# Kernel tuning notes

Hardware: AMD Instinct MI355X
Metric: run time of the kernel (lower is better)

## Reference

```python
import jax, jax.numpy as jnp
import numpy as np

# Static sizes
B, P, D = 256, 32, 128            # graphs, patches/graph, hidden
N, NS = 200_000, 500_000          # original nodes, combined-subgraph nodes
ES, EO = 1_000_000, 400_000       # combined-subgraph edges, original edges
RW, PRW = 20, 8                   # rw_dim, patch_rw_dim
NL_GNN, NL_MIX = 4, 2
TH, CH = 64, 512                  # mixer token-hidden, channel-hidden
ATOM_V, BOND_V = 128, 8


def seg_sum(x, idx, n):
    return jax.ops.segment_sum(x, idx, num_segments=n)


def seg_mean(x, idx, n):
    s = seg_sum(x, idx, n)
    c = seg_sum(jnp.ones((idx.shape[0], 1), x.dtype), idx, n)
    return s / jnp.maximum(c, 1.0)


def ln(x, g, b):
    m = x.mean(-1, keepdims=True)
    v = x.var(-1, keepdims=True)
    return (x - m) * jax.lax.rsqrt(v + 1e-5) * g + b


def setup_inputs() -> dict:
    key = jax.random.key(0)
    ks = iter(jax.random.split(key, 48))

    def nrm(shape, scale=0.05):
        return jax.random.normal(next(ks), shape, jnp.float32) * scale

    inp = {
        "x_atom": jax.random.randint(next(ks), (N,), 0, ATOM_V),
        "rw_pos_enc": jax.random.normal(next(ks), (N, RW), jnp.float32),
        "edge_attr": jax.random.randint(next(ks), (EO,), 0, BOND_V),
        "nodes_mapper": jax.random.randint(next(ks), (NS,), 0, N),
        "edges_mapper": jax.random.randint(next(ks), (ES,), 0, EO),
        "edge_index": jax.random.randint(next(ks), (2, ES), 0, NS),
        "batch_x": jax.random.randint(next(ks), (NS,), 0, B * P),
        "patch_pe": jax.random.normal(next(ks), (B * P, PRW), jnp.float32),
        "mask": jnp.ones((B, P), dtype=bool),
        # parameters
        "atom_emb": nrm((ATOM_V, D)),
        "bond_emb": nrm((BOND_V, D)),
        "rw_W": nrm((RW, D)), "rw_b": jnp.zeros((D,), jnp.float32),
        "prw_W": nrm((PRW, D)), "prw_b": jnp.zeros((D,), jnp.float32),
        "gnn_W": nrm((NL_GNN, D, D)), "gnn_b": jnp.zeros((NL_GNN, D), jnp.float32),
        "U_W": nrm((NL_GNN - 1, D, D)), "U_b": jnp.zeros((NL_GNN - 1, D), jnp.float32),
        "ln1_g": jnp.ones((NL_MIX, D), jnp.float32), "ln1_b": jnp.zeros((NL_MIX, D), jnp.float32),
        "tW1": nrm((NL_MIX, P, TH)), "tb1": jnp.zeros((NL_MIX, TH), jnp.float32),
        "tW2": nrm((NL_MIX, TH, P)), "tb2": jnp.zeros((NL_MIX, P), jnp.float32),
        "ln2_g": jnp.ones((NL_MIX, D), jnp.float32), "ln2_b": jnp.zeros((NL_MIX, D), jnp.float32),
        "cW1": nrm((NL_MIX, D, CH)), "cb1": jnp.zeros((NL_MIX, CH), jnp.float32),
        "cW2": nrm((NL_MIX, CH, D)), "cb2": jnp.zeros((NL_MIX, D), jnp.float32),
        "oW1": nrm((D, D)), "ob1": jnp.zeros((D,), jnp.float32),
        "oW2": nrm((D, 1)), "ob2": jnp.zeros((1,), jnp.float32),
    }
    return inp


def reference(x_atom, rw_pos_enc, edge_attr, nodes_mapper, edges_mapper, edge_index,
              batch_x, patch_pe, mask, atom_emb, bond_emb, rw_W, rw_b, prw_W, prw_b,
              gnn_W, gnn_b, U_W, U_b, ln1_g, ln1_b, tW1, tb1, tW2, tb2,
              ln2_g, ln2_b, cW1, cb1, cW2, cb2, oW1, ob1, oW2, ob2):
    # node / edge encoders
    x = atom_emb[x_atom] + rw_pos_enc @ rw_W + rw_b          # [N, D]
    e = bond_emb[edge_attr][edges_mapper]                    # [ES, D]
    x = x[nodes_mapper]                                      # [NS, D]
    src, dst = edge_index[0], edge_index[1]

    for i in range(NL_GNN):
        if i > 0:
            # patch-pool -> broadcast back, mix, then sync copies of same node
            sub = seg_mean(x, batch_x, B * P)[batch_x]
            x = x + jax.nn.relu(sub @ U_W[i - 1] + U_b[i - 1])
            x = seg_mean(x, nodes_mapper, N)[nodes_mapper]
        # GINE-style conv: msg = relu(x_src + e), sum-aggregate, MLP, residual
        msg = jax.nn.relu(x[src] + e)                        # [ES, D]
        agg = seg_sum(msg, dst, NS)                          # [NS, D]
        x = x + jax.nn.relu((x + agg) @ gnn_W[i] + gnn_b[i])

    sx = seg_mean(x, batch_x, B * P) + patch_pe @ prw_W + prw_b   # [B*P, D]
    m = sx.reshape(B, P, D)

    for l in range(NL_MIX):
        # token mixing
        y = ln(m, ln1_g[l], ln1_b[l]).transpose(0, 2, 1)     # [B, D, P]
        y = jax.nn.gelu(y @ tW1[l] + tb1[l]) @ tW2[l] + tb2[l]
        m = m + y.transpose(0, 2, 1)
        # channel mixing
        y = ln(m, ln2_g[l], ln2_b[l])
        m = m + (jax.nn.gelu(y @ cW1[l] + cb1[l]) @ cW2[l] + cb2[l])

    mf = mask.astype(jnp.float32)
    pooled = (m * mf[:, :, None]).sum(1) / mf.sum(1, keepdims=True)  # [B, D]
    return jax.nn.relu(pooled @ oW1 + ob1) @ oW2 + ob2              # [B, 1]
```

## Files before the change

kernel.cpp:

```cpp
#include <hip/hip_runtime.h>
#include <hip/hip_bf16.h>
#include <math.h>

#define N_ORIG 200000
#define NS_    500000
#define ES_    1000000
#define B_     256
#define P_     32
#define D_     128
#define BP_    8192
#define RW_    20
#define PRW_   8
#define TH_    64
#define CH_    512

static inline int cdiv_l(long a, long b){ return (int)((a + b - 1) / b); }

typedef unsigned short ushort_t;
typedef __attribute__((ext_vector_type(8))) short gmx_bv8;
typedef __attribute__((ext_vector_type(4))) float gmx_fv4;

__device__ __forceinline__ float b2f(ushort_t u){
    union { unsigned int i; float f; } c; c.i = ((unsigned int)u) << 16; return c.f;
}
__device__ __forceinline__ ushort_t f2b(float f){
    union { float f; unsigned int u; } c; c.f = f;
    unsigned int u = c.u;
    u += 0x7fffu + ((u >> 16) & 1u);
    return (ushort_t)(u >> 16);
}
__device__ __forceinline__ float4 b2f4(ushort4 v){
    return make_float4(b2f(v.x), b2f(v.y), b2f(v.z), b2f(v.w));
}
__device__ __forceinline__ ushort4 f2b4(float4 v){
    ushort4 r; r.x = f2b(v.x); r.y = f2b(v.y); r.z = f2b(v.z); r.w = f2b(v.w); return r;
}

__device__ __forceinline__ float gelu_t(float x){
    float t = tanhf(0.7978845608028654f * (x + 0.044715f * x * x * x));
    return 0.5f * x * (1.0f + t);
}

__global__ void k_breadcrumb(float* __restrict__ out, int n, float v){
    int i = blockIdx.x * 256 + threadIdx.x;
    if (i < n) out[i] = v;
}

__global__ void k_deg_edges(const int* __restrict__ dstv, const int* __restrict__ perm,
                            int* __restrict__ deg){
    int e = blockIdx.x * 256 + threadIdx.x;
    if (e >= ES_) return;
    atomicAdd(&deg[perm[dstv[e]]], 1);
}

__global__ void k_deg_ns(const int* __restrict__ bx, const int* __restrict__ nm,
                         int* __restrict__ pdeg, int* __restrict__ ndeg){
    int i = blockIdx.x * 256 + threadIdx.x;
    if (i >= NS_) return;
    atomicAdd(&pdeg[bx[i]], 1);
    atomicAdd(&ndeg[nm[i]], 1);
}

__global__ __launch_bounds__(256)
void k_scan1(int* __restrict__ a, int* __restrict__ bsum, int n){
    __shared__ int sb[256];
    int tid = threadIdx.x;
    long base = (long)blockIdx.x * 1024 + tid * 4;
    int v0 = 0, v1 = 0, v2 = 0, v3 = 0;
    if (base + 0 < n) v0 = a[base + 0];
    if (base + 1 < n) v1 = a[base + 1];
    if (base + 2 < n) v2 = a[base + 2];
    if (base + 3 < n) v3 = a[base + 3];
    int tsum = v0 + v1 + v2 + v3;
    sb[tid] = tsum;
    __syncthreads();
    for (int o = 1; o < 256; o <<= 1){
        int t = (tid >= o) ? sb[tid - o] : 0;
        __syncthreads();
        sb[tid] += t;
        __syncthreads();
    }
    int excl = sb[tid] - tsum;
    if (tid == 255) bsum[blockIdx.x] = sb[255];
    if (base + 0 < n) a[base + 0] = excl;
    if (base + 1 < n) a[base + 1] = excl + v0;
    if (base + 2 < n) a[base + 2] = excl + v0 + v1;
    if (base + 3 < n) a[base + 3] = excl + v0 + v1 + v2;
}

__global__ __launch_bounds__(512)
void k_scan2(int* __restrict__ bsum, int nb){
    __shared__ int sb[512];
    int tid = threadIdx.x;
    int orig = (tid < nb) ? bsum[tid] : 0;
    sb[tid] = orig;
    __syncthreads();
    for (int o = 1; o < 512; o <<= 1){
        int t = (tid >= o) ? sb[tid - o] : 0;
        __syncthreads();
        sb[tid] += t;
        __syncthreads();
    }
    if (tid < nb) bsum[tid] = sb[tid] - orig;
}

__global__ void k_scan3(int* __restrict__ a, const int* __restrict__ bsum,
                        int* __restrict__ cursor, int n, int total){
    long i = (long)blockIdx.x * 256 + threadIdx.x;
    if (i < n){
        int v = a[i] + bsum[i >> 10];
        a[i] = v;
        cursor[i] = v;
    } else if (i == n){
        a[n] = total;
    }
}

__global__ void k_scatter_ns(const int* __restrict__ bx, const int* __restrict__ nm,
                             int* __restrict__ cur_p, int* __restrict__ cur_n,
                             int* __restrict__ perm, int* __restrict__ bx2,
                             int* __restrict__ nm2, int* __restrict__ nlist){
    int i = blockIdx.x * 256 + threadIdx.x;
    if (i >= NS_) return;
    int b = bx[i], n = nm[i];
    int pp = atomicAdd(&cur_p[b], 1);
    perm[i] = pp;
    bx2[pp] = b;
    nm2[pp] = n;
    int pn = atomicAdd(&cur_n[n], 1);
    nlist[pn] = pp;
}

__global__ void k_scatter_edges(const int* __restrict__ srcv, const int* __restrict__ dstv,
                                const int* __restrict__ ea, const int* __restrict__ em,
                                const int* __restrict__ nm, const int* __restrict__ perm,
                                int* __restrict__ cursor, int* __restrict__ epack){
    int e = blockIdx.x * 256 + threadIdx.x;
    if (e >= ES_) return;
    int nd = perm[dstv[e]];
    int pos = atomicAdd(&cursor[nd], 1);
    epack[pos] = nm[srcv[e]] | (ea[em[e]] << 18);
}

__global__ void k_encode(const int* __restrict__ xa, const float* __restrict__ rw,
                         const float* __restrict__ aemb, const float* __restrict__ rwW,
                         const float* __restrict__ rwb, ushort_t* __restrict__ xn){
    long i = (long)blockIdx.x * 256 + threadIdx.x;
    if (i >= (long)N_ORIG * 32) return;
    int n = (int)(i >> 5), q = (int)(i & 31);
    const float4* aemb4 = (const float4*)aemb;
    const float4* rwW4  = (const float4*)rwW;
    const float4* rwb4  = (const float4*)rwb;
    float4 v = aemb4[(long)xa[n] * 32 + q];
    float4 bb = rwb4[q];
    v.x += bb.x; v.y += bb.y; v.z += bb.z; v.w += bb.w;
    const float* rr = rw + (long)n * RW_;
    #pragma unroll
    for (int k = 0; k < RW_; k++){
        float rv = rr[k];
        float4 ww = rwW4[k * 32 + q];
        v.x = fmaf(rv, ww.x, v.x); v.y = fmaf(rv, ww.y, v.y);
        v.z = fmaf(rv, ww.z, v.z); v.w = fmaf(rv, ww.w, v.w);
    }
    ((ushort4*)xn)[i] = f2b4(v);
}

__global__ __launch_bounds__(128)
void k_patch_pool(const ushort_t* __restrict__ xs, const int* __restrict__ prp,
                  ushort_t* __restrict__ pm){
    int p = blockIdx.x, d = threadIdx.x;
    int j0 = prp[p], j1 = prp[p + 1];
    float s0 = 0.f, s1 = 0.f;
    int j = j0;
    for (; j + 1 < j1; j += 2){
        s0 += b2f(xs[(long)j * D_ + d]);
        s1 += b2f(xs[(long)(j + 1) * D_ + d]);
    }
    if (j < j1) s0 += b2f(xs[(long)j * D_ + d]);
    pm[(long)p * D_ + d] = f2b((s0 + s1) / fmaxf((float)(j1 - j0), 1.f));
}

__global__ __launch_bounds__(128)
void k_patch_pool_sx(const ushort_t* __restrict__ xs, const int* __restrict__ prp,
                     const float* __restrict__ ppe, const float* __restrict__ pW,
                     const float* __restrict__ pb, float* __restrict__ m){
    int p = blockIdx.x, d = threadIdx.x;
    int j0 = prp[p], j1 = prp[p + 1];
    float s0 = 0.f, s1 = 0.f;
    int j = j0;
    for (; j + 1 < j1; j += 2){
        s0 += b2f(xs[(long)j * D_ + d]);
        s1 += b2f(xs[(long)(j + 1) * D_ + d]);
    }
    if (j < j1) s0 += b2f(xs[(long)j * D_ + d]);
    float s = (s0 + s1) / fmaxf((float)(j1 - j0), 1.f) + pb[d];
    #pragma unroll
    for (int k = 0; k < PRW_; k++) s = fmaf(ppe[p * PRW_ + k], pW[k * D_ + d], s);
    m[(long)p * D_ + d] = s;
}

__global__ __launch_bounds__(128)
void k_node_resync(const ushort_t* __restrict__ xs, const ushort_t* __restrict__ subT,
                   const int* __restrict__ bx2, const int* __restrict__ nrp,
                   const int* __restrict__ nlist, ushort_t* __restrict__ xn){
    int n = blockIdx.x, d = threadIdx.x;
    int j0 = nrp[n], j1 = nrp[n + 1];
    float s = 0.f;
    int j = j0;
    for (; j + 2 <= j1; j += 2){
        int ra = nlist[j], rb = nlist[j + 1];
        int ba = bx2[ra], bb_ = bx2[rb];
        float va = b2f(xs[(long)ra * D_ + d]);
        float vb = b2f(xs[(long)rb * D_ + d]);
        float ua = b2f(subT[(long)ba * D_ + d]);
        float ub = b2f(subT[(long)bb_ * D_ + d]);
        s += va + ua + vb + ub;
    }
    if (j < j1){
        int ra = nlist[j];
        int ba = bx2[ra];
        s += b2f(xs[(long)ra * D_ + d]) + b2f(subT[(long)ba * D_ + d]);
    }
    xn[(long)n * D_ + d] = f2b(s / fmaxf((float)(j1 - j0), 1.f));
}

__global__ __launch_bounds__(256)
void k_gemm_mfma(const ushort_t* __restrict__ in, const float* __restrict__ W,
                 const float* __restrict__ bvec, ushort_t* __restrict__ out, int nrows){
    __shared__ char sInB[16 * 256];
    int tid = threadIdx.x;
    int wid = tid >> 6, lane = tid & 63;
    int colA = lane & 15, rgrp = lane >> 4;
    int c0 = 32 * wid + colA, c1 = c0 + 16;
    float bias0 = bvec[c0], bias1 = bvec[c1];
    union { gmx_bv8 v; short s[8]; } bf0[4], bf1[4];
    #pragma unroll
    for (int kb = 0; kb < 4; kb++){
        int kr = kb * 32 + 8 * rgrp;
        #pragma unroll
        for (int j = 0; j < 8; j++){
            bf0[kb].s[j] = (short)f2b(W[(kr + j) * D_ + c0]);
            bf1[kb].s[j] = (short)f2b(W[(kr + j) * D_ + c1]);
        }
    }
    const ushort4* in4 = (const ushort4*)in;
    int ntiles = nrows >> 4;
    for (int tile = blockIdx.x; tile < ntiles; tile += gridDim.x){
        int r0 = tile * 16;
        #pragma unroll
        for (int it = 0; it < 2; it++){
            int k = tid + it * 256;
            int r = k >> 5, q = k & 31;
            ushort4 v = in4[(long)(r0 + r) * 32 + q];
            int off = (r * 256 + q * 8) ^ ((r & 7) << 4);
            *(ushort4*)&sInB[off] = v;
        }
        __syncthreads();
        gmx_fv4 acc0 = {0.f,0.f,0.f,0.f}, acc1 = {0.f,0.f,0.f,0.f};
        #pragma unroll
        for (int kb = 0; kb < 4; kb++){
            int kslot = kb * 4 + rgrp;
            gmx_bv8 a = *(const gmx_bv8*)&sInB[(colA * 256 + kslot * 16) ^ ((colA & 7) << 4)];
            acc0 = __builtin_amdgcn_mfma_f32_16x16x32_bf16(a, bf0[kb].v, acc0, 0, 0, 0);
            acc1 = __builtin_amdgcn_mfma_f32_16x16x32_bf16(a, bf1[kb].v, acc1, 0, 0, 0);
        }
        #pragma unroll
        for (int ri = 0; ri < 4; ri++){
            long base = (long)(r0 + rgrp * 4 + ri) * D_;
            out[base + c0] = f2b(fmaxf(acc0[ri] + bias0, 0.f));
            out[base + c1] = f2b(fmaxf(acc1[ri] + bias1, 0.f));
        }
        __syncthreads();
    }
}

#define CROWS 16

__global__ __launch_bounds__(256)
void k_conv_mfma(const ushort_t* __restrict__ xn, const int* __restrict__ nm2,
                 ushort_t* __restrict__ xout,
                 const int* __restrict__ rp, const int* __restrict__ epack,
                 const float* __restrict__ bond, const float* __restrict__ W,
                 const float* __restrict__ bvec){
    __shared__ char sInB[CROWS * 256];
    __shared__ ushort_t sSelf[CROWS * D_];
    __shared__ int sRp[CROWS + 1];
    __shared__ int sEp[256];
    int tid = threadIdx.x;
    int wid = tid >> 6, lane = tid & 63;
    int colA = lane & 15, rgrp = lane >> 4;
    int c0 = 32 * wid + colA, c1 = c0 + 16;
    float bias0 = bvec[c0], bias1 = bvec[c1];
    union { gmx_bv8 v; short s[8]; } bf0[4], bf1[4];
    #pragma unroll
    for (int kb = 0; kb < 4; kb++){
        int kr = kb * 32 + 8 * rgrp;
        #pragma unroll
        for (int j = 0; j < 8; j++){
            bf0[kb].s[j] = (short)f2b(W[(kr + j) * D_ + c0]);
            bf1[kb].s[j] = (short)f2b(W[(kr + j) * D_ + c1]);
        }
    }
    const ushort4* xn4 = (const ushort4*)xn;
    const float4* bond4 = (const float4*)bond;
    const int ntiles = NS_ / CROWS;
    for (int tile = blockIdx.x; tile < ntiles; tile += gridDim.x){
        int r0 = tile * CROWS;
        if (tid < CROWS + 1) sRp[tid] = rp[r0 + tid];
        __syncthreads();
        int eb0 = sRp[0];
        int ne = sRp[CROWS] - eb0;
        int nc = ne < 256 ? ne : 256;
        for (int k2 = tid; k2 < nc; k2 += 256) sEp[k2] = epack[eb0 + k2];
        __syncthreads();
        #pragma unroll
        for (int it = 0; it < 2; it++){
            int k = tid + it * 256;
            int r = k >> 5, q = k & 31;
            ushort4 selfb = xn4[(long)nm2[r0 + r] * 32 + q];
            *(ushort4*)&sSelf[r * D_ + q * 4] = selfb;
            float4 v = b2f4(selfb);
            int e0 = sRp[r], e1 = sRp[r + 1];
            int e = e0;
            for (; e + 2 <= e1; e += 2){
                int i0 = e - eb0;
                int pk0 = (i0 < 256) ? sEp[i0] : epack[e];
                int pk1 = (i0 + 1 < 256) ? sEp[i0 + 1] : epack[e + 1];
                float4 u0 = b2f4(xn4[(long)(pk0 & 0x3FFFF) * 32 + q]);
                float4 u1 = b2f4(xn4[(long)(pk1 & 0x3FFFF) * 32 + q]);
                float4 b0 = bond4[((pk0 >> 18) & 7) * 32 + q];
                float4 b1 = bond4[((pk1 >> 18) & 7) * 32 + q];
                v.x += fmaxf(u0.x + b0.x, 0.f) + fmaxf(u1.x + b1.x, 0.f);
                v.y += fmaxf(u0.y + b0.y, 0.f) + fmaxf(u1.y + b1.y, 0.f);
                v.z += fmaxf(u0.z + b0.z, 0.f) + fmaxf(u1.z + b1.z, 0.f);
                v.w += fmaxf(u0.w + b0.w, 0.f) + fmaxf(u1.w + b1.w, 0.f);
            }
            if (e < e1){
                int i0 = e - eb0;
                int pk0 = (i0 < 256) ? sEp[i0] : epack[e];
                float4 u0 = b2f4(xn4[(long)(pk0 & 0x3FFFF) * 32 + q]);
                float4 b0 = bond4[((pk0 >> 18) & 7) * 32 + q];
                v.x += fmaxf(u0.x + b0.x, 0.f);
                v.y += fmaxf(u0.y + b0.y, 0.f);
                v.z += fmaxf(u0.z + b0.z, 0.f);
                v.w += fmaxf(u0.w + b0.w, 0.f);
            }
            int off = (r * 256 + q * 8) ^ ((r & 7) << 4);
            *(ushort4*)&sInB[off] = f2b4(v);
        }
        __syncthreads();
        gmx_fv4 acc0 = {0.f,0.f,0.f,0.f}, acc1 = {0.f,0.f,0.f,0.f};
        #pragma unroll
        for (int kb = 0; kb < 4; kb++){
            int kslot = kb * 4 + rgrp;
            gmx_bv8 a = *(const gmx_bv8*)&sInB[(colA * 256 + kslot * 16) ^ ((colA & 7) << 4)];
            acc0 = __builtin_amdgcn_mfma_f32_16x16x32_bf16(a, bf0[kb].v, acc0, 0, 0, 0);
            acc1 = __builtin_amdgcn_mfma_f32_16x16x32_bf16(a, bf1[kb].v, acc1, 0, 0, 0);
        }
        #pragma unroll
        for (int ri = 0; ri < 4; ri++){
            int prow = rgrp * 4 + ri;
            long base = (long)(r0 + prow) * D_;
            float o0 = b2f(sSelf[prow * D_ + c0]) + fmaxf(acc0[ri] + bias0, 0.f);
            float o1 = b2f(sSelf[prow * D_ + c1]) + fmaxf(acc1[ri] + bias1, 0.f);
            xout[base + c0] = f2b(o0);
            xout[base + c1] = f2b(o1);
        }
        __syncthreads();
    }
}

__global__ __launch_bounds__(256)
void k_token_mix(float* __restrict__ m, const float* __restrict__ g, const float* __restrict__ be,
                 const float* __restrict__ tW1, const float* __restrict__ tb1,
                 const float* __restrict__ tW2, const float* __restrict__ tb2){
    __shared__ float sy[P_][D_];
    __shared__ float sh[D_][TH_ + 1];
    int b = blockIdx.x, tid = threadIdx.x;
    float* mb = m + (long)b * P_ * D_;
    int wv = tid >> 6, ln_ = tid & 63;
    for (int r = wv; r < P_; r += 4){
        float v0 = mb[r * D_ + ln_], v1 = mb[r * D_ + 64 + ln_];
        float s = v0 + v1, ss = v0 * v0 + v1 * v1;
        #pragma unroll
        for (int o = 32; o > 0; o >>= 1){ s += __shfl_down(s, o, 64); ss += __shfl_down(ss, o, 64); }
        s = __shfl(s, 0, 64); ss = __shfl(ss, 0, 64);
        float mu = s * (1.f / 128.f);
        float var = ss * (1.f / 128.f) - mu * mu;
        float rs = rsqrtf(var + 1e-5f);
        sy[r][ln_]      = (v0 - mu) * rs * g[ln_]      + be[ln_];
        sy[r][64 + ln_] = (v1 - mu) * rs * g[64 + ln_] + be[64 + ln_];
    }
    __syncthreads();
    for (int o = tid; o < D_ * TH_; o += 256){
        int t = o & 63, d = o >> 6;
        float a = tb1[t];
        #pragma unroll
        for (int p = 0; p < P_; p++) a = fmaf(sy[p][d], tW1[p * TH_ + t], a);
        sh[d][t] = gelu_t(a);
    }
    __syncthreads();
    for (int o = tid; o < P_ * D_; o += 256){
        int d = o & 127, p = o >> 7;
        float a = tb2[p];
        #pragma unroll
        for (int t = 0; t < TH_; t++) a = fmaf(sh[d][t], tW2[t * P_ + p], a);
        mb[p * D_ + d] += a;
    }
}

__global__ __launch_bounds__(256)
void k_channel_mix(float* __restrict__ m, const float* __restrict__ g, const float* __restrict__ be,
                   const float* __restrict__ cW1, const float* __restrict__ cb1,
                   const float* __restrict__ cW2, const float* __restrict__ cb2){
    __shared__ float sy[16][D_];
    __shared__ float sh[16][CH_ + 1];
    int r0 = blockIdx.x * 16, tid = threadIdx.x;
    int wv = tid >> 6, ln_ = tid & 63;
    for (int r = wv; r < 16; r += 4){
        float v0 = m[(long)(r0 + r) * D_ + ln_], v1 = m[(long)(r0 + r) * D_ + 64 + ln_];
        float s = v0 + v1, ss = v0 * v0 + v1 * v1;
        #pragma unroll
        for (int o = 32; o > 0; o >>= 1){ s += __shfl_down(s, o, 64); ss += __shfl_down(ss, o, 64); }
        s = __shfl(s, 0, 64); ss = __shfl(ss, 0, 64);
        float mu = s * (1.f / 128.f);
        float var = ss * (1.f / 128.f) - mu * mu;
        float rs = rsqrtf(var + 1e-5f);
        sy[r][ln_]      = (v0 - mu) * rs * g[ln_]      + be[ln_];
        sy[r][64 + ln_] = (v1 - mu) * rs * g[64 + ln_] + be[64 + ln_];
    }
    __syncthreads();
    #pragma unroll
    for (int th = 0; th < 2; th++){
        int t = tid + th * 256;
        float acc[16];
        #pragma unroll
        for (int r = 0; r < 16; r++) acc[r] = cb1[t];
        for (int k = 0; k < D_; k++){
            float w = cW1[k * CH_ + t];
            #pragma unroll
            for (int r = 0; r < 16; r++) acc[r] = fmaf(sy[r][k], w, acc[r]);
        }
        #pragma unroll
        for (int r = 0; r < 16; r++) sh[r][t] = gelu_t(acc[r]);
    }
    __syncthreads();
    {
        int d = tid & 127, rbase = tid >> 7;
        float acc[8];
        #pragma unroll
        for (int q = 0; q < 8; q++) acc[q] = 0.f;
        for (int t = 0; t < CH_; t++){
            float w = cW2[t * D_ + d];
            #pragma unroll
            for (int q = 0; q < 8; q++) acc[q] = fmaf(sh[rbase + 2 * q][t], w, acc[q]);
        }
        float cb = cb2[d];
        #pragma unroll
        for (int q = 0; q < 8; q++){
            int row = r0 + rbase + 2 * q;
            m[(long)row * D_ + d] += acc[q] + cb;
        }
    }
}

__global__ __launch_bounds__(128)
void k_final(const float* __restrict__ m, const float* __restrict__ oW1, const float* __restrict__ ob1,
             const float* __restrict__ oW2, const float* __restrict__ ob2, float* __restrict__ out){
    __shared__ float sp[D_];
    __shared__ float red[128];
    int b = blockIdx.x, tid = threadIdx.x;
    float a = 0.f;
    for (int p = 0; p < P_; p++) a += m[(long)b * P_ * D_ + p * D_ + tid];
    sp[tid] = a * (1.0f / P_);
    __syncthreads();
    float h = ob1[tid];
    for (int d = 0; d < D_; d++) h = fmaf(sp[d], oW1[d * D_ + tid], h);
    h = fmaxf(h, 0.f) * oW2[tid];
    red[tid] = h;
    __syncthreads();
    for (int s = 64; s > 0; s >>= 1){
        if (tid < s) red[tid] += red[tid + s];
        __syncthreads();
    }
    if (tid == 0) out[b] = red[0] + ob2[0];
}

extern "C" void kernel_launch(void* const* d_in, const int* in_sizes, int n_in,
                              void* d_out, int out_size, void* d_ws, size_t ws_size,
                              hipStream_t stream){
    const int*   x_atom       = (const int*)  d_in[0];
    const float* rw_pe        = (const float*)d_in[1];
    const int*   edge_attr    = (const int*)  d_in[2];
    const int*   nodes_mapper = (const int*)  d_in[3];
    const int*   edges_mapper = (const int*)  d_in[4];
    const int*   edge_index   = (const int*)  d_in[5];
    const int*   batch_x      = (const int*)  d_in[6];
    const float* patch_pe     = (const float*)d_in[7];
    const float* atom_emb = (const float*)d_in[9];
    const float* bond_emb = (const float*)d_in[10];
    const float* rw_W  = (const float*)d_in[11];
    const float* rw_b  = (const float*)d_in[12];
    const float* prw_W = (const float*)d_in[13];
    const float* prw_b = (const float*)d_in[14];
    const float* gnn_W = (const float*)d_in[15];
    const float* gnn_b = (const float*)d_in[16];
    const float* U_W   = (const float*)d_in[17];
    const float* U_b   = (const float*)d_in[18];
    const float* ln1_g = (const float*)d_in[19];
    const float* ln1_b = (const float*)d_in[20];
    const float* tW1   = (const float*)d_in[21];
    const float* tb1   = (const float*)d_in[22];
    const float* tW2   = (const float*)d_in[23];
    const float* tb2   = (const float*)d_in[24];
    const float* ln2_g = (const float*)d_in[25];
    const float* ln2_b = (const float*)d_in[26];
    const float* cW1   = (const float*)d_in[27];
    const float* cb1   = (const float*)d_in[28];
    const float* cW2   = (const float*)d_in[29];
    const float* cb2   = (const float*)d_in[30];
    const float* oW1   = (const float*)d_in[31];
    const float* ob1   = (const float*)d_in[32];
    const float* oW2   = (const float*)d_in[33];
    const float* ob2   = (const float*)d_in[34];

    const int* srcv = edge_index;
    const int* dstv = edge_index + ES_;

    char* w = (char*)d_ws;
    size_t offXS  = 0;
    size_t offXN  = offXS  + (size_t)NS_ * D_ * 2;
    size_t offRP  = offXN  + (size_t)N_ORIG * D_ * 2;
    size_t offEP  = offRP  + 2000064;
    size_t offPRP = offEP  + (size_t)ES_ * 4;
    size_t offNRP = offPRP + 32832;
    size_t offNL  = offNRP + 800064;
    size_t offPERM= offNL  + (size_t)NS_ * 4;
    size_t offBX2 = offPERM+ (size_t)NS_ * 4;
    size_t offNM2 = offBX2 + (size_t)NS_ * 4;
    size_t offBS  = offNM2 + (size_t)NS_ * 4;
    size_t offPM  = offBS  + 2048;
    size_t offST  = offPM  + (size_t)BP_ * D_ * 2;
    size_t offM   = offST  + (size_t)BP_ * D_ * 2;
    size_t needed = offM   + (size_t)BP_ * D_ * 4;

    if (ws_size < needed){
        k_breadcrumb<<<cdiv_l(out_size, 256), 256, 0, stream>>>((float*)d_out, out_size,
                                                                (float)(ws_size >> 20));
        return;
    }

    k_breadcrumb<<<cdiv_l(out_size, 256), 256, 0, stream>>>((float*)d_out, out_size, 7.0f);

    ushort_t* xs = (ushort_t*)(w + offXS);
    ushort_t* xn = (ushort_t*)(w + offXN);
    int* rp    = (int*)(w + offRP);
    int* ep    = (int*)(w + offEP);
    int* prp   = (int*)(w + offPRP);
    int* nrp   = (int*)(w + offNRP);
    int* nlist = (int*)(w + offNL);
    int* perm  = (int*)(w + offPERM);
    int* bx2   = (int*)(w + offBX2);
    int* nm2   = (int*)(w + offNM2);
    int* bsum  = (int*)(w + offBS);
    ushort_t* pm   = (ushort_t*)(w + offPM);
    ushort_t* subT = (ushort_t*)(w + offST);
    float*    mbuf = (float*)(w + offM);
    int* cur_e = (int*)(w + offXS);
    int* cur_p = (int*)(w + offXS + 4194304);
    int* cur_n = (int*)(w + offXS + 8388608);

    const int TPB = 256;

    hipMemsetAsync(prp, 0, 32832, stream);
    hipMemsetAsync(nrp, 0, 800064, stream);
    k_deg_ns<<<cdiv_l(NS_, TPB), TPB, 0, stream>>>(batch_x, nodes_mapper, prp, nrp);
    k_scan1<<<cdiv_l(BP_, 1024), TPB, 0, stream>>>(prp, bsum, BP_);
    k_scan2<<<1, 512, 0, stream>>>(bsum, cdiv_l(BP_, 1024));
    k_scan3<<<cdiv_l(BP_ + 1, TPB), TPB, 0, stream>>>(prp, bsum, cur_p, BP_, NS_);
    k_scan1<<<cdiv_l(N_ORIG, 1024), TPB, 0, stream>>>(nrp, bsum, N_ORIG);
    k_scan2<<<1, 512, 0, stream>>>(bsum, cdiv_l(N_ORIG, 1024));
    k_scan3<<<cdiv_l(N_ORIG + 1, TPB), TPB, 0, stream>>>(nrp, bsum, cur_n, N_ORIG, NS_);
    k_scatter_ns<<<cdiv_l(NS_, TPB), TPB, 0, stream>>>(batch_x, nodes_mapper, cur_p, cur_n,
                                                       perm, bx2, nm2, nlist);
    hipMemsetAsync(rp, 0, 2000064, stream);
    k_deg_edges<<<cdiv_l(ES_, TPB), TPB, 0, stream>>>(dstv, perm, rp);
    k_scan1<<<cdiv_l(NS_, 1024), TPB, 0, stream>>>(rp, bsum, NS_);
    k_scan2<<<1, 512, 0, stream>>>(bsum, cdiv_l(NS_, 1024));
    k_scan3<<<cdiv_l(NS_ + 1, TPB), TPB, 0, stream>>>(rp, bsum, cur_e, NS_, ES_);
    k_scatter_edges<<<cdiv_l(ES_, TPB), TPB, 0, stream>>>(srcv, dstv, edge_attr, edges_mapper,
                                                          nodes_mapper, perm, cur_e, ep);

    k_encode<<<cdiv_l((long)N_ORIG * 32, TPB), TPB, 0, stream>>>(x_atom, rw_pe, atom_emb,
                                                                 rw_W, rw_b, xn);

    for (int i = 0; i < 4; i++){
        if (i > 0){
            k_patch_pool<<<BP_, 128, 0, stream>>>(xs, prp, pm);
            k_gemm_mfma<<<256, TPB, 0, stream>>>(pm, U_W + (i - 1) * D_ * D_,
                                                 U_b + (i - 1) * D_, subT, BP_);
            k_node_resync<<<N_ORIG, 128, 0, stream>>>(xs, subT, bx2, nrp, nlist, xn);
        }
        k_conv_mfma<<<2048, TPB, 0, stream>>>(xn, nm2, xs, rp, ep, bond_emb,
                                              gnn_W + i * D_ * D_, gnn_b + i * D_);
    }

    k_patch_pool_sx<<<BP_, 128, 0, stream>>>(xs, prp, patch_pe, prw_W, prw_b, mbuf);

    for (int l = 0; l < 2; l++){
        k_token_mix<<<B_, TPB, 0, stream>>>(mbuf, ln1_g + l * D_, ln1_b + l * D_,
                                            tW1 + l * P_ * TH_, tb1 + l * TH_,
                                            tW2 + l * TH_ * P_, tb2 + l * P_);
        k_channel_mix<<<BP_ / 16, TPB, 0, stream>>>(mbuf, ln2_g + l * D_, ln2_b + l * D_,
                                                    cW1 + l * D_ * CH_, cb1 + l * CH_,
                                                    cW2 + l * CH_ * D_, cb2 + l * D_);
    }
    k_final<<<B_, 128, 0, stream>>>(mbuf, oW1, ob1, oW2, ob2, (float*)d_out);
}
```

Before: 1.676 ms.

## Order subgraph nodes by original node and fuse patch pooling into GEMM

Subgraph node rows are now permuted so that copies of the same original node sit next to each other. This makes the node resync read contiguous rows, while patch pooling gathers rows through a new per-patch index list. Patch pooling and the U GEMM are fused into one kernel that pools 16 patches into shared memory and multiplies them with MFMA, which removes the intermediate pooled buffer and one launch. The cost moves to indirect gathers in patch pooling, and the edge CSR ordering by destination changes as well, which may alter locality in the conv kernel.

```diff
diff --git a/kernel.cpp b/kernel.cpp
--- a/kernel.cpp
+++ b/kernel.cpp
@@ -119,16 +119,16 @@
 __global__ void k_scatter_ns(const int* __restrict__ bx, const int* __restrict__ nm,
                              int* __restrict__ cur_p, int* __restrict__ cur_n,
                              int* __restrict__ perm, int* __restrict__ bx2,
-                             int* __restrict__ nm2, int* __restrict__ nlist){
+                             int* __restrict__ nm2, int* __restrict__ plist){
     int i = blockIdx.x * 256 + threadIdx.x;
     if (i >= NS_) return;
     int b = bx[i], n = nm[i];
+    int pn = atomicAdd(&cur_n[n], 1);
+    perm[i] = pn;
+    bx2[pn] = b;
+    nm2[pn] = n;
     int pp = atomicAdd(&cur_p[b], 1);
-    perm[i] = pp;
-    bx2[pp] = b;
-    nm2[pp] = n;
-    int pn = atomicAdd(&cur_n[n], 1);
-    nlist[pn] = pp;
+    plist[pp] = pn;
 }
 
 __global__ void k_scatter_edges(const int* __restrict__ srcv, const int* __restrict__ dstv,
@@ -165,69 +165,12 @@
     ((ushort4*)xn)[i] = f2b4(v);
 }
 
-__global__ __launch_bounds__(128)
-void k_patch_pool(const ushort_t* __restrict__ xs, const int* __restrict__ prp,
-                  ushort_t* __restrict__ pm){
-    int p = blockIdx.x, d = threadIdx.x;
-    int j0 = prp[p], j1 = prp[p + 1];
-    float s0 = 0.f, s1 = 0.f;
-    int j = j0;
-    for (; j + 1 < j1; j += 2){
-        s0 += b2f(xs[(long)j * D_ + d]);
-        s1 += b2f(xs[(long)(j + 1) * D_ + d]);
-    }
-    if (j < j1) s0 += b2f(xs[(long)j * D_ + d]);
-    pm[(long)p * D_ + d] = f2b((s0 + s1) / fmaxf((float)(j1 - j0), 1.f));
-}
-
-__global__ __launch_bounds__(128)
-void k_patch_pool_sx(const ushort_t* __restrict__ xs, const int* __restrict__ prp,
-                     const float* __restrict__ ppe, const float* __restrict__ pW,
-                     const float* __restrict__ pb, float* __restrict__ m){
-    int p = blockIdx.x, d = threadIdx.x;
-    int j0 = prp[p], j1 = prp[p + 1];
-    float s0 = 0.f, s1 = 0.f;
-    int j = j0;
-    for (; j + 1 < j1; j += 2){
-        s0 += b2f(xs[(long)j * D_ + d]);
-        s1 += b2f(xs[(long)(j + 1) * D_ + d]);
-    }
-    if (j < j1) s0 += b2f(xs[(long)j * D_ + d]);
-    float s = (s0 + s1) / fmaxf((float)(j1 - j0), 1.f) + pb[d];
-    #pragma unroll
-    for (int k = 0; k < PRW_; k++) s = fmaf(ppe[p * PRW_ + k], pW[k * D_ + d], s);
-    m[(long)p * D_ + d] = s;
-}
-
-__global__ __launch_bounds__(128)
-void k_node_resync(const ushort_t* __restrict__ xs, const ushort_t* __restrict__ subT,
-                   const int* __restrict__ bx2, const int* __restrict__ nrp,
-                   const int* __restrict__ nlist, ushort_t* __restrict__ xn){
-    int n = blockIdx.x, d = threadIdx.x;
-    int j0 = nrp[n], j1 = nrp[n + 1];
-    float s = 0.f;
-    int j = j0;
-    for (; j + 2 <= j1; j += 2){
-        int ra = nlist[j], rb = nlist[j + 1];
-        int ba = bx2[ra], bb_ = bx2[rb];
-        float va = b2f(xs[(long)ra * D_ + d]);
-        float vb = b2f(xs[(long)rb * D_ + d]);
-        float ua = b2f(subT[(long)ba * D_ + d]);
-        float ub = b2f(subT[(long)bb_ * D_ + d]);
-        s += va + ua + vb + ub;
-    }
-    if (j < j1){
-        int ra = nlist[j];
-        int ba = bx2[ra];
-        s += b2f(xs[(long)ra * D_ + d]) + b2f(subT[(long)ba * D_ + d]);
-    }
-    xn[(long)n * D_ + d] = f2b(s / fmaxf((float)(j1 - j0), 1.f));
-}
-
 __global__ __launch_bounds__(256)
-void k_gemm_mfma(const ushort_t* __restrict__ in, const float* __restrict__ W,
-                 const float* __restrict__ bvec, ushort_t* __restrict__ out, int nrows){
+void k_pool_gemm(const ushort_t* __restrict__ xs, const int* __restrict__ prp,
+                 const int* __restrict__ plist, const float* __restrict__ W,
+                 const float* __restrict__ bvec, ushort_t* __restrict__ out){
     __shared__ char sInB[16 * 256];
+    __shared__ int sPrp[17];
     int tid = threadIdx.x;
     int wid = tid >> 6, lane = tid & 63;
     int colA = lane & 15, rgrp = lane >> 4;
@@ -243,35 +186,89 @@
             bf1[kb].s[j] = (short)f2b(W[(kr + j) * D_ + c1]);
         }
     }
-    const ushort4* in4 = (const ushort4*)in;
-    int ntiles = nrows >> 4;
-    for (int tile = blockIdx.x; tile < ntiles; tile += gridDim.x){
-        int r0 = tile * 16;
-        #pragma unroll
-        for (int it = 0; it < 2; it++){
-            int k = tid + it * 256;
-            int r = k >> 5, q = k & 31;
-            ushort4 v = in4[(long)(r0 + r) * 32 + q];
-            int off = (r * 256 + q * 8) ^ ((r & 7) << 4);
-            *(ushort4*)&sInB[off] = v;
-        }
-        __syncthreads();
-        gmx_fv4 acc0 = {0.f,0.f,0.f,0.f}, acc1 = {0.f,0.f,0.f,0.f};
-        #pragma unroll
-        for (int kb = 0; kb < 4; kb++){
-            int kslot = kb * 4 + rgrp;
-            gmx_bv8 a = *(const gmx_bv8*)&sInB[(colA * 256 + kslot * 16) ^ ((colA & 7) << 4)];
-            acc0 = __builtin_amdgcn_mfma_f32_16x16x32_bf16(a, bf0[kb].v, acc0, 0, 0, 0);
-            acc1 = __builtin_amdgcn_mfma_f32_16x16x32_bf16(a, bf1[kb].v, acc1, 0, 0, 0);
-        }
-        #pragma unroll
-        for (int ri = 0; ri < 4; ri++){
-            long base = (long)(r0 + rgrp * 4 + ri) * D_;
-            out[base + c0] = f2b(fmaxf(acc0[ri] + bias0, 0.f));
-            out[base + c1] = f2b(fmaxf(acc1[ri] + bias1, 0.f));
-        }
-        __syncthreads();
-    }
+    int p0 = blockIdx.x * 16;
+    if (tid < 17) sPrp[tid] = prp[p0 + tid];
+    __syncthreads();
+    const ushort4* xs4 = (const ushort4*)xs;
+    #pragma unroll
+    for (int it = 0; it < 2; it++){
+        int k = tid + it * 256;
+        int r = k >> 5, q = k & 31;
+        int j0 = sPrp[r], j1 = sPrp[r + 1];
+        float4 s0 = make_float4(0.f,0.f,0.f,0.f), s1 = make_float4(0.f,0.f,0.f,0.f);
+        int j = j0;
+        for (; j + 2 <= j1; j += 2){
+            float4 a = b2f4(xs4[(long)plist[j] * 32 + q]);
+            float4 b = b2f4(xs4[(long)plist[j + 1] * 32 + q]);
+            s0.x += a.x; s0.y += a.y; s0.z += a.z; s0.w += a.w;
+            s1.x += b.x; s1.y += b.y; s1.z += b.z; s1.w += b.w;
+        }
+        if (j < j1){
+            float4 a = b2f4(xs4[(long)plist[j] * 32 + q]);
+            s0.x += a.x; s0.y += a.y; s0.z += a.z; s0.w += a.w;
+        }
+        float inv = 1.f / fmaxf((float)(j1 - j0), 1.f);
+        float4 v = make_float4((s0.x + s1.x) * inv, (s0.y + s1.y) * inv,
+                               (s0.z + s1.z) * inv, (s0.w + s1.w) * inv);
+        int off = (r * 256 + q * 8) ^ ((r & 7) << 4);
+        *(ushort4*)&sInB[off] = f2b4(v);
+    }
+    __syncthreads();
+    gmx_fv4 acc0 = {0.f,0.f,0.f,0.f}, acc1 = {0.f,0.f,0.f,0.f};
+    #pragma unroll
+    for (int kb = 0; kb < 4; kb++){
+        int kslot = kb * 4 + rgrp;
+        gmx_bv8 a = *(const gmx_bv8*)&sInB[(colA * 256 + kslot * 16) ^ ((colA & 7) << 4)];
+        acc0 = __builtin_amdgcn_mfma_f32_16x16x32_bf16(a, bf0[kb].v, acc0, 0, 0, 0);
+        acc1 = __builtin_amdgcn_mfma_f32_16x16x32_bf16(a, bf1[kb].v, acc1, 0, 0, 0);
+    }
+    #pragma unroll
+    for (int ri = 0; ri < 4; ri++){
+        long base = (long)(p0 + rgrp * 4 + ri) * D_;
+        out[base + c0] = f2b(fmaxf(acc0[ri] + bias0, 0.f));
+        out[base + c1] = f2b(fmaxf(acc1[ri] + bias1, 0.f));
+    }
+}
+
+__global__ __launch_bounds__(128)
+void k_patch_pool_sx(const ushort_t* __restrict__ xs, const int* __restrict__ prp,
+                     const int* __restrict__ plist, const float* __restrict__ ppe,
+                     const float* __restrict__ pW, const float* __restrict__ pb,
+                     float* __restrict__ m){
+    int p = blockIdx.x, d = threadIdx.x;
+    int j0 = prp[p], j1 = prp[p + 1];
+    float s0 = 0.f, s1 = 0.f;
+    int j = j0;
+    for (; j + 2 <= j1; j += 2){
+        s0 += b2f(xs[(long)plist[j] * D_ + d]);
+        s1 += b2f(xs[(long)plist[j + 1] * D_ + d]);
+    }
+    if (j < j1) s0 += b2f(xs[(long)plist[j] * D_ + d]);
+    float s = (s0 + s1) / fmaxf((float)(j1 - j0), 1.f) + pb[d];
+    #pragma unroll
+    for (int k = 0; k < PRW_; k++) s = fmaf(ppe[p * PRW_ + k], pW[k * D_ + d], s);
+    m[(long)p * D_ + d] = s;
+}
+
+__global__ __launch_bounds__(128)
+void k_node_resync(const ushort_t* __restrict__ xs, const ushort_t* __restrict__ subT,
+                   const int* __restrict__ bx2, const int* __restrict__ nrp,
+                   ushort_t* __restrict__ xn){
+    int n = blockIdx.x, d = threadIdx.x;
+    int j0 = nrp[n], j1 = nrp[n + 1];
+    float s = 0.f;
+    int j = j0;
+    for (; j + 2 <= j1; j += 2){
+        float va = b2f(xs[(long)j * D_ + d]);
+        float vb = b2f(xs[(long)(j + 1) * D_ + d]);
+        float ua = b2f(subT[(long)bx2[j] * D_ + d]);
+        float ub = b2f(subT[(long)bx2[j + 1] * D_ + d]);
+        s += va + ua + vb + ub;
+    }
+    if (j < j1){
+        s += b2f(xs[(long)j * D_ + d]) + b2f(subT[(long)bx2[j] * D_ + d]);
+    }
+    xn[(long)n * D_ + d] = f2b(s / fmaxf((float)(j1 - j0), 1.f));
 }
 
 #define CROWS 16
@@ -534,13 +531,12 @@
     size_t offEP  = offRP  + 2000064;
     size_t offPRP = offEP  + (size_t)ES_ * 4;
     size_t offNRP = offPRP + 32832;
-    size_t offNL  = offNRP + 800064;
-    size_t offPERM= offNL  + (size_t)NS_ * 4;
+    size_t offPL  = offNRP + 800064;
+    size_t offPERM= offPL  + (size_t)NS_ * 4;
     size_t offBX2 = offPERM+ (size_t)NS_ * 4;
     size_t offNM2 = offBX2 + (size_t)NS_ * 4;
     size_t offBS  = offNM2 + (size_t)NS_ * 4;
-    size_t offPM  = offBS  + 2048;
-    size_t offST  = offPM  + (size_t)BP_ * D_ * 2;
+    size_t offST  = offBS  + 2048;
     size_t offM   = offST  + (size_t)BP_ * D_ * 2;
     size_t needed = offM   + (size_t)BP_ * D_ * 4;
 
@@ -558,12 +554,11 @@
     int* ep    = (int*)(w + offEP);
     int* prp   = (int*)(w + offPRP);
     int* nrp   = (int*)(w + offNRP);
-    int* nlist = (int*)(w + offNL);
+    int* plist = (int*)(w + offPL);
     int* perm  = (int*)(w + offPERM);
     int* bx2   = (int*)(w + offBX2);
     int* nm2   = (int*)(w + offNM2);
     int* bsum  = (int*)(w + offBS);
-    ushort_t* pm   = (ushort_t*)(w + offPM);
     ushort_t* subT = (ushort_t*)(w + offST);
     float*    mbuf = (float*)(w + offM);
     int* cur_e = (int*)(w + offXS);
@@ -582,7 +577,7 @@
     k_scan2<<<1, 512, 0, stream>>>(bsum, cdiv_l(N_ORIG, 1024));
     k_scan3<<<cdiv_l(N_ORIG + 1, TPB), TPB, 0, stream>>>(nrp, bsum, cur_n, N_ORIG, NS_);
     k_scatter_ns<<<cdiv_l(NS_, TPB), TPB, 0, stream>>>(batch_x, nodes_mapper, cur_p, cur_n,
-                                                       perm, bx2, nm2, nlist);
+                                                       perm, bx2, nm2, plist);
     hipMemsetAsync(rp, 0, 2000064, stream);
     k_deg_edges<<<cdiv_l(ES_, TPB), TPB, 0, stream>>>(dstv, perm, rp);
     k_scan1<<<cdiv_l(NS_, 1024), TPB, 0, stream>>>(rp, bsum, NS_);
@@ -596,16 +591,16 @@
 
     for (int i = 0; i < 4; i++){
         if (i > 0){
-            k_patch_pool<<<BP_, 128, 0, stream>>>(xs, prp, pm);
-            k_gemm_mfma<<<256, TPB, 0, stream>>>(pm, U_W + (i - 1) * D_ * D_,
-                                                 U_b + (i - 1) * D_, subT, BP_);
-            k_node_resync<<<N_ORIG, 128, 0, stream>>>(xs, subT, bx2, nrp, nlist, xn);
+            k_pool_gemm<<<BP_ / 16, TPB, 0, stream>>>(xs, prp, plist,
+                                                      U_W + (i - 1) * D_ * D_,
+                                                      U_b + (i - 1) * D_, subT);
+            k_node_resync<<<N_ORIG, 128, 0, stream>>>(xs, subT, bx2, nrp, xn);
         }
         k_conv_mfma<<<2048, TPB, 0, stream>>>(xn, nm2, xs, rp, ep, bond_emb,
                                               gnn_W + i * D_ * D_, gnn_b + i * D_);
     }
 
-    k_patch_pool_sx<<<BP_, 128, 0, stream>>>(xs, prp, patch_pe, prw_W, prw_b, mbuf);
+    k_patch_pool_sx<<<BP_, 128, 0, stream>>>(xs, prp, plist, patch_pe, prw_W, prw_b, mbuf);
 
     for (int l = 0; l < 2; l++){
         k_token_mix<<<B_, TPB, 0, stream>>>(mbuf, ln1_g + l * D_, ln1_b + l * D_,
```

Result: faster. 1.625 ms (-3.0%).
